# Optimization experiments

Measured on AMD Instinct MI355X. Metric: run time of the kernel, lower is better.

The kernel has to match this reference:

```python
import jax, jax.numpy as jnp
import numpy as np

N_NODES = 100000
N_EDGES = 1600000
D_FEAT = 128
N_CLASSES = 64


def setup_inputs() -> dict:
    key = jax.random.key(0)
    k1, k2, k3, k4 = jax.random.split(key, 4)
    x = jax.random.normal(k1, (N_NODES, D_FEAT), dtype=jnp.float32)
    edge_index = jax.random.randint(k2, (2, N_EDGES), 0, N_NODES, dtype=jnp.int32)
    # Linear(num_features -> num_classes) params (torch stores W as [out, in])
    W = jax.random.normal(k3, (N_CLASSES, D_FEAT), dtype=jnp.float32) * (1.0 / np.sqrt(D_FEAT))
    b = jax.random.normal(k4, (N_CLASSES,), dtype=jnp.float32) * 0.01
    return {"x": x, "edge_index": edge_index, "W": W, "b": b}


def reference(x, edge_index, W, b):
    N = x.shape[0]
    idx = jnp.arange(N, dtype=edge_index.dtype)
    # gcn_norm with add_self_loops=True: A_hat = A + I, sym-normalized
    src = jnp.concatenate([edge_index[0], idx])  # message sources
    dst = jnp.concatenate([edge_index[1], idx])  # aggregation targets
    deg = jax.ops.segment_sum(jnp.ones_like(dst, dtype=x.dtype), dst, num_segments=N)
    dinv = jnp.where(deg > 0, jax.lax.rsqrt(deg), jnp.zeros_like(deg))
    norm = dinv[src] * dinv[dst]  # [E+N]
    # K=1 propagation: gather, weight, scatter-add
    h = jax.ops.segment_sum(x[src] * norm[:, None], dst, num_segments=N)  # [N, F]
    logits = h @ W.T + b  # [N, C]
    return jax.nn.log_softmax(logits, axis=1)
```

## Files before the change

### kernel.cpp

```cpp
#include <hip/hip_runtime.h>
#include <hip/hip_bf16.h>
#include <hip/hip_fp16.h>
#include <math.h>

#define N_NODES   100000
#define N_EDGES   1600000
#define D_FEAT    128
#define N_CLASSES 64

#define BKT_SHIFT 7
#define BKT_NODES 128
#define NB        782
#define CAP       2560
#define CHUNK     8192
#define NBLK_A    ((N_EDGES + CHUNK - 1) / CHUNK)
#define GROWS     128
#define NBLK_G    ((N_NODES + GROWS - 1) / GROWS)

#define OFF_BCNT   400384
#define OFF_BINNED 404480
#define OFF_ZP     8412160

typedef __attribute__((ext_vector_type(8))) short bf16x8;
typedef __attribute__((ext_vector_type(4))) float f32x4;
typedef __attribute__((ext_vector_type(4))) unsigned int u32x4;

static __device__ inline unsigned f2bf1(float f) {
    unsigned u = __float_as_uint(f);
    return (u + 0x7FFF + ((u >> 16) & 1)) >> 16;
}
static __device__ inline unsigned pack2(float a, float b) {
    return f2bf1(a) | (f2bf1(b) << 16);
}
static __device__ inline float2 h2f2(unsigned u) {
    __half2 h = *(__half2*)&u;
    return __half22float2(h);
}

__global__ __launch_bounds__(1024) void bin_kernel(const int* __restrict__ src,
                                                   const int* __restrict__ dst,
                                                   int* __restrict__ bcnt,
                                                   int* __restrict__ binned) {
    __shared__ int hist[NB];
    __shared__ int rbase[NB];
    __shared__ int loc[NB];
    __shared__ int wsum[16];
    __shared__ int dbuf[CHUNK];
    __shared__ int sbuf[CHUNK];

    const int tid  = threadIdx.x;
    const int lane = tid & 63;
    const int wid  = tid >> 6;
    const int e0 = blockIdx.x * CHUNK;
    const int e1 = min(e0 + CHUNK, N_EDGES);
    const int n  = e1 - e0;

    if (tid < NB) hist[tid] = 0;
    __syncthreads();

    for (int i = tid; i < n; i += 1024) {
        int d = dst[e0 + i];
        dbuf[i] = d;
        atomicAdd(&hist[d >> BKT_SHIFT], 1);
    }
    __syncthreads();

    int x = (tid < NB) ? hist[tid] : 0;
    int sc = x;
#pragma unroll
    for (int off = 1; off < 64; off <<= 1) {
        int t = __shfl_up(sc, off, 64);
        if (lane >= off) sc += t;
    }
    if (lane == 63) wsum[wid] = sc;
    __syncthreads();
    if (tid < 16) {
        int w  = wsum[tid];
        int ws = w;
#pragma unroll
        for (int off = 1; off < 16; off <<= 1) {
            int t = __shfl_up(ws, off, 16);
            if (tid >= off) ws += t;
        }
        wsum[tid] = ws - w;
    }
    __syncthreads();
    if (tid < NB) {
        loc[tid] = sc - x + wsum[wid];
        if (x) rbase[tid] = atomicAdd(&bcnt[tid], x);
        hist[tid] = 0;
    }
    __syncthreads();

    for (int i = tid; i < n; i += 1024) {
        int d   = dbuf[i];
        int sv  = src[e0 + i];
        int bkt = d >> BKT_SHIFT;
        int p   = atomicAdd(&hist[bkt], 1);
        sbuf[loc[bkt] + p] = (sv << BKT_SHIFT) | (d & (BKT_NODES - 1));
    }
    __syncthreads();

    const int g16 = lane >> 4;
    const int l16 = lane & 15;
    for (int b2 = wid * 4 + g16; b2 < NB; b2 += 64) {
        const int len = hist[b2];
        if (!len) continue;
        const int st = loc[b2];
        const int rb = rbase[b2];
        for (int k = l16; k < len; k += 16) {
            const int off = rb + k;
            if (off < CAP)
                binned[b2 * CAP + off] = sbuf[st + k];
        }
    }
}

__global__ __launch_bounds__(1024) void sortdeg_kernel(const int* __restrict__ bcnt,
                                                       int* __restrict__ binned,
                                                       int* __restrict__ meta) {
    __shared__ int buf[CAP];
    __shared__ int hcnt[BKT_NODES];
    __shared__ int cur[BKT_NODES];
    __shared__ int rowstart[BKT_NODES + 1];

    const int tid  = threadIdx.x;
    const int lane = tid & 63;
    const int wid  = tid >> 6;

    if (tid < BKT_NODES) { hcnt[tid] = 0; cur[tid] = 0; }
    __syncthreads();

    const int n    = min(bcnt[blockIdx.x], CAP);
    const int base = blockIdx.x * CAP;

    for (int i = tid; i < n; i += 1024) {
        int v = binned[base + i];
        buf[i] = v;
        atomicAdd(&hcnt[v & (BKT_NODES - 1)], 1);
    }
    __syncthreads();

    if (wid == 0) {
        int v0 = hcnt[lane];
        int v1 = hcnt[64 + lane];
        int s0 = v0;
#pragma unroll
        for (int off = 1; off < 64; off <<= 1) {
            int t = __shfl_up(s0, off, 64);
            if (lane >= off) s0 += t;
        }
        int tot0 = __shfl(s0, 63, 64);
        int s1 = v1;
#pragma unroll
        for (int off = 1; off < 64; off <<= 1) {
            int t = __shfl_up(s1, off, 64);
            if (lane >= off) s1 += t;
        }
        s1 += tot0;
        if (lane == 0) rowstart[0] = 0;
        rowstart[1 + lane]  = s0;
        rowstart[65 + lane] = s1;
    }
    __syncthreads();

    for (int i = tid; i < n; i += 1024) {
        int v  = buf[i];
        int nd = v & (BKT_NODES - 1);
        int p  = atomicAdd(&cur[nd], 1);
        binned[base + rowstart[nd] + p] = v >> BKT_SHIFT;
    }

    if (tid < BKT_NODES) {
        int node = blockIdx.x * BKT_NODES + tid;
        if (node < N_NODES) {
            int st = base + rowstart[tid];
            int dg = min(hcnt[tid], 2047);
            meta[node] = st | (dg << 21);
        }
    }
}

__global__ __launch_bounds__(256) void gemm_kernel(const float* __restrict__ x,
                                                   const float* __restrict__ W,
                                                   const int* __restrict__ meta,
                                                   __half* __restrict__ zp) {
    __shared__ short Wb[64 * 136];
    const int tid  = threadIdx.x;

    const float4* __restrict__ W4 = (const float4*)W;
    for (int idx = tid; idx < 64 * 32; idx += 256) {
        int nn = idx >> 5, k4 = idx & 31;
        float4 v = W4[idx];
        uint2 p;
        p.x = pack2(v.x, v.y);
        p.y = pack2(v.z, v.w);
        *(uint2*)&Wb[nn * 136 + k4 * 4] = p;
    }
    __syncthreads();

    const int lane = tid & 63;
    const int wv   = tid >> 6;
    const int m    = lane & 15;
    const int half = lane >> 4;

    bf16x8 bfr[4][4];
#pragma unroll
    for (int t = 0; t < 4; t++)
#pragma unroll
        for (int j = 0; j < 4; j++)
            bfr[t][j] = *(bf16x8*)&Wb[(j * 16 + m) * 136 + t * 32 + half * 8];

#pragma unroll
    for (int rt = 0; rt < 2; rt++) {
        const int row0 = blockIdx.x * GROWS + rt * 64;
        const int arow = min(row0 + wv * 16 + m, N_NODES - 1);
        const float4* __restrict__ xr = (const float4*)&x[arow * D_FEAT];

        f32x4 acc[4];
#pragma unroll
        for (int j = 0; j < 4; j++) acc[j] = (f32x4){0.f, 0.f, 0.f, 0.f};

#pragma unroll
        for (int t = 0; t < 4; t++) {
            const float4 p0 = xr[t * 8 + half * 2];
            const float4 p1 = xr[t * 8 + half * 2 + 1];
            union { bf16x8 v; unsigned u[4]; } au;
            au.u[0] = pack2(p0.x, p0.y);
            au.u[1] = pack2(p0.z, p0.w);
            au.u[2] = pack2(p1.x, p1.y);
            au.u[3] = pack2(p1.z, p1.w);
#pragma unroll
            for (int j = 0; j < 4; j++)
                acc[j] = __builtin_amdgcn_mfma_f32_16x16x32_bf16(au.v, bfr[t][j], acc[j], 0, 0, 0);
        }

#pragma unroll
        for (int r = 0; r < 4; r++) {
            const int row = row0 + wv * 16 + half * 4 + r;
            if (row < N_NODES) {
                const int dg = ((unsigned)meta[row]) >> 21;
                const float dinv = rsqrtf((float)(dg + 1));
#pragma unroll
                for (int j = 0; j < 4; j++)
                    zp[row * N_CLASSES + j * 16 + m] = __float2half(acc[j][r] * dinv);
            }
        }
    }
}

__global__ __launch_bounds__(256) void agg_kernel(const int* __restrict__ meta,
                                                  const int* __restrict__ binned,
                                                  const __half* __restrict__ zp,
                                                  const float* __restrict__ b,
                                                  float* __restrict__ out) {
    const int wid  = threadIdx.x >> 6;
    const int lane = threadIdx.x & 63;
    const int half = lane >> 5;
    const int l31  = lane & 31;
    const int sub  = (lane >> 3) & 3;
    const int o8   = (lane & 7) * 8;

    const int nodeA = blockIdx.x * 8 + wid * 2;
    const int node  = nodeA + half;

    const unsigned mvA = (unsigned)meta[nodeA];
    const unsigned mvB = (unsigned)meta[nodeA + 1];
    const int cA = mvA >> 21;
    const int cB = mvB >> 21;
    const int st  = half ? (int)(mvB & 0x1FFFFF) : (int)(mvA & 0x1FFFFF);
    const int cnt = half ? cB : cA;
    const int cmax = max(cA, cB);

    float a[8] = {0.f, 0.f, 0.f, 0.f, 0.f, 0.f, 0.f, 0.f};
    for (int base = 0; base < cmax; base += 32) {
        const int bn = cnt - base;
        const int idxoff = max(min(l31, bn - 1), 0);
        int sv = binned[st + base + idxoff];
        if (bn <= 0) sv = 0;
        const int jn = min(cmax - base, 32);
        const int jm = (jn + 3) >> 2;
        for (int j = 0; j < jm; j++) {
            const int eid = j * 4 + sub;
            const int srcl = (half << 5) + max(min(eid, bn - 1), 0);
            const int row = __shfl(sv, srcl, 64);
            const u32x4 g = *(const u32x4*)&zp[row * N_CLASSES + o8];
            if (eid < bn) {
#pragma unroll
                for (int k = 0; k < 4; k++) {
                    float2 f = h2f2(g[k]);
                    a[2 * k]     += f.x;
                    a[2 * k + 1] += f.y;
                }
            }
        }
    }
#pragma unroll
    for (int mask = 8; mask <= 16; mask <<= 1)
#pragma unroll
        for (int k = 0; k < 8; k++)
            a[k] += __shfl_xor(a[k], mask, 64);

    const u32x4 sg = *(const u32x4*)&zp[node * N_CLASSES + o8];
#pragma unroll
    for (int k = 0; k < 4; k++) {
        float2 f = h2f2(sg[k]);
        a[2 * k]     += f.x;
        a[2 * k + 1] += f.y;
    }

    const float dinv = rsqrtf((float)(cnt + 1));
    float v[8];
#pragma unroll
    for (int k = 0; k < 8; k++) v[k] = a[k] * dinv + b[o8 + k];

    float m = v[0];
#pragma unroll
    for (int k = 1; k < 8; k++) m = fmaxf(m, v[k]);
#pragma unroll
    for (int mask = 1; mask <= 4; mask <<= 1)
        m = fmaxf(m, __shfl_xor(m, mask, 64));
    float l = 0.f;
#pragma unroll
    for (int k = 0; k < 8; k++) l += __expf(v[k] - m);
#pragma unroll
    for (int mask = 1; mask <= 4; mask <<= 1)
        l += __shfl_xor(l, mask, 64);
    const float lg = m + __logf(l);

    if (sub == 0) {
        float4 o0, o1;
        o0.x = v[0] - lg; o0.y = v[1] - lg; o0.z = v[2] - lg; o0.w = v[3] - lg;
        o1.x = v[4] - lg; o1.y = v[5] - lg; o1.z = v[6] - lg; o1.w = v[7] - lg;
        *(float4*)&out[node * N_CLASSES + o8]     = o0;
        *(float4*)&out[node * N_CLASSES + o8 + 4] = o1;
    }
}

extern "C" void kernel_launch(void* const* d_in, const int* in_sizes, int n_in,
                              void* d_out, int out_size, void* d_ws, size_t ws_size,
                              hipStream_t stream) {
    const float* x    = (const float*)d_in[0];
    const int*   edge = (const int*)d_in[1];
    const float* W    = (const float*)d_in[2];
    const float* b    = (const float*)d_in[3];
    float* out = (float*)d_out;

    char* ws = (char*)d_ws;
    int*    meta   = (int*)(ws);
    int*    bcnt   = (int*)(ws + OFF_BCNT);
    int*    binned = (int*)(ws + OFF_BINNED);
    __half* zp     = (__half*)(ws + OFF_ZP);

    const int* srcv = edge;
    const int* dstv = edge + N_EDGES;

    hipMemsetAsync(bcnt, 0, NB * sizeof(int), stream);
    bin_kernel<<<NBLK_A, 1024, 0, stream>>>(srcv, dstv, bcnt, binned);
    sortdeg_kernel<<<NB, 1024, 0, stream>>>(bcnt, binned, meta);
    gemm_kernel<<<NBLK_G, 256, 0, stream>>>(x, W, meta, zp);
    agg_kernel<<<N_NODES / 8, 256, 0, stream>>>(meta, binned, zp, b, out);
}
```

Baseline: 169.2 us.

## Move per-bucket sort into aggregation kernel and accumulate gathers in half2

Result: no change. 169.4 us (+0.2%).

```diff
diff --git a/kernel.cpp b/kernel.cpp
--- a/kernel.cpp
+++ b/kernel.cpp
@@ -35,6 +35,12 @@
 static __device__ inline float2 h2f2(unsigned u) {
     __half2 h = *(__half2*)&u;
     return __half22float2(h);
+}
+static __device__ inline unsigned hadd2u(unsigned a, unsigned b) {
+    __half2 ha = *(__half2*)&a;
+    __half2 hb = *(__half2*)&b;
+    __half2 r  = __hadd2(ha, hb);
+    return *(unsigned*)&r;
 }
 
 __global__ __launch_bounds__(1024) void bin_kernel(const int* __restrict__ src,
@@ -116,74 +122,29 @@
     }
 }
 
-__global__ __launch_bounds__(1024) void sortdeg_kernel(const int* __restrict__ bcnt,
-                                                       int* __restrict__ binned,
-                                                       int* __restrict__ meta) {
-    __shared__ int buf[CAP];
+__global__ __launch_bounds__(256) void deg_kernel(const int* __restrict__ bcnt,
+                                                  const int* __restrict__ binned,
+                                                  int* __restrict__ deg) {
     __shared__ int hcnt[BKT_NODES];
-    __shared__ int cur[BKT_NODES];
-    __shared__ int rowstart[BKT_NODES + 1];
-
-    const int tid  = threadIdx.x;
-    const int lane = tid & 63;
-    const int wid  = tid >> 6;
-
-    if (tid < BKT_NODES) { hcnt[tid] = 0; cur[tid] = 0; }
+    const int tid = threadIdx.x;
+    if (tid < BKT_NODES) hcnt[tid] = 0;
     __syncthreads();
 
     const int n    = min(bcnt[blockIdx.x], CAP);
     const int base = blockIdx.x * CAP;
-
-    for (int i = tid; i < n; i += 1024) {
-        int v = binned[base + i];
-        buf[i] = v;
-        atomicAdd(&hcnt[v & (BKT_NODES - 1)], 1);
-    }
-    __syncthreads();
-
-    if (wid == 0) {
-        int v0 = hcnt[lane];
-        int v1 = hcnt[64 + lane];
-        int s0 = v0;
-#pragma unroll
-        for (int off = 1; off < 64; off <<= 1) {
-            int t = __shfl_up(s0, off, 64);
-            if (lane >= off) s0 += t;
-        }
-        int tot0 = __shfl(s0, 63, 64);
-        int s1 = v1;
-#pragma unroll
-        for (int off = 1; off < 64; off <<= 1) {
-            int t = __shfl_up(s1, off, 64);
-            if (lane >= off) s1 += t;
-        }
-        s1 += tot0;
-        if (lane == 0) rowstart[0] = 0;
-        rowstart[1 + lane]  = s0;
-        rowstart[65 + lane] = s1;
-    }
-    __syncthreads();
-
-    for (int i = tid; i < n; i += 1024) {
-        int v  = buf[i];
-        int nd = v & (BKT_NODES - 1);
-        int p  = atomicAdd(&cur[nd], 1);
-        binned[base + rowstart[nd] + p] = v >> BKT_SHIFT;
-    }
+    for (int i = tid; i < n; i += 256)
+        atomicAdd(&hcnt[binned[base + i] & (BKT_NODES - 1)], 1);
+    __syncthreads();
 
     if (tid < BKT_NODES) {
         int node = blockIdx.x * BKT_NODES + tid;
-        if (node < N_NODES) {
-            int st = base + rowstart[tid];
-            int dg = min(hcnt[tid], 2047);
-            meta[node] = st | (dg << 21);
-        }
+        if (node < N_NODES) deg[node] = hcnt[tid];
     }
 }
 
 __global__ __launch_bounds__(256) void gemm_kernel(const float* __restrict__ x,
                                                    const float* __restrict__ W,
-                                                   const int* __restrict__ meta,
+                                                   const int* __restrict__ deg,
                                                    __half* __restrict__ zp) {
     __shared__ short Wb[64 * 136];
     const int tid  = threadIdx.x;
@@ -239,7 +200,7 @@
         for (int r = 0; r < 4; r++) {
             const int row = row0 + wv * 16 + half * 4 + r;
             if (row < N_NODES) {
-                const int dg = ((unsigned)meta[row]) >> 21;
+                const int dg = deg[row];
                 const float dinv = rsqrtf((float)(dg + 1));
 #pragma unroll
                 for (int j = 0; j < 4; j++)
@@ -249,91 +210,134 @@
     }
 }
 
-__global__ __launch_bounds__(256) void agg_kernel(const int* __restrict__ meta,
-                                                  const int* __restrict__ binned,
-                                                  const __half* __restrict__ zp,
-                                                  const float* __restrict__ b,
-                                                  float* __restrict__ out) {
-    const int wid  = threadIdx.x >> 6;
-    const int lane = threadIdx.x & 63;
+__global__ __launch_bounds__(1024) void agg_kernel(const int* __restrict__ bcnt,
+                                                   const int* __restrict__ binned,
+                                                   const __half* __restrict__ zp,
+                                                   const float* __restrict__ b,
+                                                   float* __restrict__ out) {
+    __shared__ int buf[CAP];
+    __shared__ int sorted[CAP];
+    __shared__ int hcnt[BKT_NODES];
+    __shared__ int cur[BKT_NODES];
+    __shared__ int rowstart[BKT_NODES];
+
+    const int tid  = threadIdx.x;
+    const int lane = tid & 63;
+    const int wid  = tid >> 6;
+
+    if (tid < BKT_NODES) { hcnt[tid] = 0; cur[tid] = 0; }
+    __syncthreads();
+
+    const int bkt  = blockIdx.x;
+    const int n    = min(bcnt[bkt], CAP);
+    const int base = bkt * CAP;
+
+    for (int i = tid; i < n; i += 1024) {
+        int v = binned[base + i];
+        buf[i] = v;
+        atomicAdd(&hcnt[v & (BKT_NODES - 1)], 1);
+    }
+    __syncthreads();
+
+    if (wid == 0) {
+        int v0 = hcnt[lane];
+        int v1 = hcnt[64 + lane];
+        int s0 = v0;
+#pragma unroll
+        for (int off = 1; off < 64; off <<= 1) {
+            int t = __shfl_up(s0, off, 64);
+            if (lane >= off) s0 += t;
+        }
+        int tot0 = __shfl(s0, 63, 64);
+        int s1 = v1;
+#pragma unroll
+        for (int off = 1; off < 64; off <<= 1) {
+            int t = __shfl_up(s1, off, 64);
+            if (lane >= off) s1 += t;
+        }
+        rowstart[lane]      = s0 - v0;
+        rowstart[64 + lane] = s1 + tot0 - v1;
+    }
+    __syncthreads();
+
+    for (int i = tid; i < n; i += 1024) {
+        int v  = buf[i];
+        int nd = v & (BKT_NODES - 1);
+        int p  = atomicAdd(&cur[nd], 1);
+        sorted[rowstart[nd] + p] = v >> BKT_SHIFT;
+    }
+    __syncthreads();
+
     const int half = lane >> 5;
-    const int l31  = lane & 31;
     const int sub  = (lane >> 3) & 3;
     const int o8   = (lane & 7) * 8;
 
-    const int nodeA = blockIdx.x * 8 + wid * 2;
-    const int node  = nodeA + half;
-
-    const unsigned mvA = (unsigned)meta[nodeA];
-    const unsigned mvB = (unsigned)meta[nodeA + 1];
-    const int cA = mvA >> 21;
-    const int cB = mvB >> 21;
-    const int st  = half ? (int)(mvB & 0x1FFFFF) : (int)(mvA & 0x1FFFFF);
-    const int cnt = half ? cB : cA;
-    const int cmax = max(cA, cB);
-
-    float a[8] = {0.f, 0.f, 0.f, 0.f, 0.f, 0.f, 0.f, 0.f};
-    for (int base = 0; base < cmax; base += 32) {
-        const int bn = cnt - base;
-        const int idxoff = max(min(l31, bn - 1), 0);
-        int sv = binned[st + base + idxoff];
-        if (bn <= 0) sv = 0;
-        const int jn = min(cmax - base, 32);
-        const int jm = (jn + 3) >> 2;
-        for (int j = 0; j < jm; j++) {
-            const int eid = j * 4 + sub;
-            const int srcl = (half << 5) + max(min(eid, bn - 1), 0);
-            const int row = __shfl(sv, srcl, 64);
-            const u32x4 g = *(const u32x4*)&zp[row * N_CLASSES + o8];
-            if (eid < bn) {
-#pragma unroll
-                for (int k = 0; k < 4; k++) {
-                    float2 f = h2f2(g[k]);
-                    a[2 * k]     += f.x;
-                    a[2 * k + 1] += f.y;
-                }
-            }
-        }
-    }
-#pragma unroll
-    for (int mask = 8; mask <= 16; mask <<= 1)
-#pragma unroll
-        for (int k = 0; k < 8; k++)
-            a[k] += __shfl_xor(a[k], mask, 64);
-
-    const u32x4 sg = *(const u32x4*)&zp[node * N_CLASSES + o8];
-#pragma unroll
-    for (int k = 0; k < 4; k++) {
-        float2 f = h2f2(sg[k]);
-        a[2 * k]     += f.x;
-        a[2 * k + 1] += f.y;
-    }
-
-    const float dinv = rsqrtf((float)(cnt + 1));
-    float v[8];
-#pragma unroll
-    for (int k = 0; k < 8; k++) v[k] = a[k] * dinv + b[o8 + k];
-
-    float m = v[0];
-#pragma unroll
-    for (int k = 1; k < 8; k++) m = fmaxf(m, v[k]);
-#pragma unroll
-    for (int mask = 1; mask <= 4; mask <<= 1)
-        m = fmaxf(m, __shfl_xor(m, mask, 64));
-    float l = 0.f;
-#pragma unroll
-    for (int k = 0; k < 8; k++) l += __expf(v[k] - m);
-#pragma unroll
-    for (int mask = 1; mask <= 4; mask <<= 1)
-        l += __shfl_xor(l, mask, 64);
-    const float lg = m + __logf(l);
-
-    if (sub == 0) {
-        float4 o0, o1;
-        o0.x = v[0] - lg; o0.y = v[1] - lg; o0.z = v[2] - lg; o0.w = v[3] - lg;
-        o1.x = v[4] - lg; o1.y = v[5] - lg; o1.z = v[6] - lg; o1.w = v[7] - lg;
-        *(float4*)&out[node * N_CLASSES + o8]     = o0;
-        *(float4*)&out[node * N_CLASSES + o8 + 4] = o1;
+#pragma unroll 1
+    for (int pass = 0; pass < 4; pass++) {
+        const int nl   = pass * 32 + wid * 2 + half;
+        const int node = bkt * BKT_NODES + nl;
+        const int cnt  = hcnt[nl];
+        const int st   = rowstart[nl];
+
+        float a8[8] = {0.f, 0.f, 0.f, 0.f, 0.f, 0.f, 0.f, 0.f};
+        for (int be = 0; be < cnt; be += 64) {
+            const int en = min(cnt - be, 64);
+            unsigned p2[4] = {0u, 0u, 0u, 0u};
+            for (int e = sub; e < en; e += 4) {
+                const int row = sorted[st + be + e];
+                const u32x4 g = *(const u32x4*)&zp[row * N_CLASSES + o8];
+#pragma unroll
+                for (int k = 0; k < 4; k++) p2[k] = hadd2u(p2[k], g[k]);
+            }
+#pragma unroll
+            for (int k = 0; k < 4; k++) {
+                float2 f = h2f2(p2[k]);
+                a8[2 * k]     += f.x;
+                a8[2 * k + 1] += f.y;
+            }
+        }
+#pragma unroll
+        for (int mask = 8; mask <= 16; mask <<= 1)
+#pragma unroll
+            for (int k = 0; k < 8; k++)
+                a8[k] += __shfl_xor(a8[k], mask, 64);
+
+        if (node < N_NODES) {
+            const u32x4 sg = *(const u32x4*)&zp[node * N_CLASSES + o8];
+#pragma unroll
+            for (int k = 0; k < 4; k++) {
+                float2 f = h2f2(sg[k]);
+                a8[2 * k]     += f.x;
+                a8[2 * k + 1] += f.y;
+            }
+
+            const float dinv = rsqrtf((float)(cnt + 1));
+            float v[8];
+#pragma unroll
+            for (int k = 0; k < 8; k++) v[k] = a8[k] * dinv + b[o8 + k];
+
+            float m = v[0];
+#pragma unroll
+            for (int k = 1; k < 8; k++) m = fmaxf(m, v[k]);
+#pragma unroll
+            for (int mask = 1; mask <= 4; mask <<= 1)
+                m = fmaxf(m, __shfl_xor(m, mask, 64));
+            float l = 0.f;
+#pragma unroll
+            for (int k = 0; k < 8; k++) l += __expf(v[k] - m);
+#pragma unroll
+            for (int mask = 1; mask <= 4; mask <<= 1)
+                l += __shfl_xor(l, mask, 64);
+            const float lg = m + __logf(l);
+
+            if (sub == 0) {
+                float4 o0, o1;
+                o0.x = v[0] - lg; o0.y = v[1] - lg; o0.z = v[2] - lg; o0.w = v[3] - lg;
+                o1.x = v[4] - lg; o1.y = v[5] - lg; o1.z = v[6] - lg; o1.w = v[7] - lg;
+                *(float4*)&out[node * N_CLASSES + o8]     = o0;
+                *(float4*)&out[node * N_CLASSES + o8 + 4] = o1;
+            }
+        }
     }
 }
 
@@ -347,7 +351,7 @@
     float* out = (float*)d_out;
 
     char* ws = (char*)d_ws;
-    int*    meta   = (int*)(ws);
+    int*    deg    = (int*)(ws);
     int*    bcnt   = (int*)(ws + OFF_BCNT);
     int*    binned = (int*)(ws + OFF_BINNED);
     __half* zp     = (__half*)(ws + OFF_ZP);
@@ -357,7 +361,7 @@
 
     hipMemsetAsync(bcnt, 0, NB * sizeof(int), stream);
     bin_kernel<<<NBLK_A, 1024, 0, stream>>>(srcv, dstv, bcnt, binned);
-    sortdeg_kernel<<<NB, 1024, 0, stream>>>(bcnt, binned, meta);
-    gemm_kernel<<<NBLK_G, 256, 0, stream>>>(x, W, meta, zp);
-    agg_kernel<<<N_NODES / 8, 256, 0, stream>>>(meta, binned, zp, b, out);
-}
+    deg_kernel<<<NB, 256, 0, stream>>>(bcnt, binned, deg);
+    gemm_kernel<<<NBLK_G, 256, 0, stream>>>(x, W, deg, zp);
+    agg_kernel<<<NB, 1024, 0, stream>>>(bcnt, binned, zp, b, out);
+}
```
